# Optimization experiments

Hardware: AMD Instinct MI355X
Metric: run time of the kernel (lower is better)

The kernel has to match this reference:

```python
import jax, jax.numpy as jnp
import numpy as np

N, E, D, H1, H2 = 50000, 800000, 128, 128, 128


def setup_inputs() -> dict:
    key = jax.random.key(0)
    ks = jax.random.split(key, 9)
    s = 0.05
    return {
        "x": jax.random.normal(ks[0], (N, D), dtype=jnp.float32),
        "edge_index": jax.random.randint(ks[1], (2, E), 0, N, dtype=jnp.int64),
        "W_l1": jax.random.normal(ks[2], (D, H1), dtype=jnp.float32) * s,
        "b_l1": jnp.zeros((H1,), dtype=jnp.float32),
        "W_r1": jax.random.normal(ks[3], (D, H1), dtype=jnp.float32) * s,
        "W_l2": jax.random.normal(ks[4], (H1, H2), dtype=jnp.float32) * s,
        "b_l2": jnp.zeros((H2,), dtype=jnp.float32),
        "W_r2": jax.random.normal(ks[5], (H1, H2), dtype=jnp.float32) * s,
        "W_e": jax.random.normal(ks[6], (2 * H2, 1), dtype=jnp.float32) * s,
        "b_e": jnp.zeros((1,), dtype=jnp.float32),
    }


def _sage_conv(h, src, tgt, n_nodes, W_l, b_l, W_r):
    # PyG SAGEConv (mean aggr): out = lin_l(mean_{j in N(i)} h_j) + lin_r(h_i)
    msg = h[src]                                              # [E, F] gather
    agg = jax.ops.segment_sum(msg, tgt, num_segments=n_nodes)  # [N, F]
    cnt = jax.ops.segment_sum(jnp.ones((src.shape[0], 1), h.dtype), tgt,
                              num_segments=n_nodes)            # [N, 1]
    mean = agg / jnp.maximum(cnt, 1.0)                         # empty nbrs -> 0
    return mean @ W_l + b_l + h @ W_r


def reference(x, edge_index, W_l1, b_l1, W_r1, W_l2, b_l2, W_r2, W_e, b_e):
    src, tgt = edge_index[0], edge_index[1]
    n_nodes = x.shape[0]
    h = jax.nn.relu(_sage_conv(x, src, tgt, n_nodes, W_l1, b_l1, W_r1))
    # dropout is identity in eval mode
    h = _sage_conv(h, src, tgt, n_nodes, W_l2, b_l2, W_r2)
    z = jnp.concatenate([h[src], h[tgt]], axis=-1)  # [E, 2*H2]
    y = z @ W_e + b_e                                # [E, 1]
    return jax.nn.sigmoid(y)
```

## Files before the change

kernel.cpp:

```cpp
#include <hip/hip_runtime.h>

#define NN 50000
#define NE 800000
#define DD 128
#define BUCKETS 196
#define PB 4096
#define PBLK 196
#define EMAX 6144
#define BPAD 264
#define PACKB 6250
#define WTB 128

typedef unsigned int uint_t;
typedef unsigned short ush_t;
typedef __attribute__((ext_vector_type(8))) short short8;
typedef __attribute__((ext_vector_type(4))) float f32x4;

__device__ __forceinline__ float bflo(uint_t u) { return __uint_as_float(u << 16); }
__device__ __forceinline__ float bfhi(uint_t u) { return __uint_as_float(u & 0xffff0000u); }
__device__ __forceinline__ ush_t f2bf(float f) {
  uint_t u = __float_as_uint(f);
  u += 0x7fffu + ((u >> 16) & 1u);
  return (ush_t)(u >> 16);
}
__device__ __forceinline__ uint_t pack2(float a, float b) {
  return (uint_t)f2bf(a) | ((uint_t)f2bf(b) << 16);
}

__device__ __forceinline__ int ld_idx(const void* ei, int is64, long long i) {
  return is64 ? (int)((const long long*)ei)[i] : ((const int*)ei)[i];
}

__device__ __forceinline__ int detect64(const void* ei) {
  const unsigned long long* p = (const unsigned long long*)ei;
  unsigned long long w = p[threadIdx.x & 63];
  return __ballot((w >> 32) != 0) == 0ull ? 1 : 0;
}

__device__ __forceinline__ int block_incl_scan(int v, int tid, int* wsum) {
  int lane = tid & 63, wave = tid >> 6;
  int s = v;
#pragma unroll
  for (int off = 1; off < 64; off <<= 1) {
    int u = __shfl_up(s, off, 64);
    if (lane >= off) s += u;
  }
  if (lane == 63) wsum[wave] = s;
  __syncthreads();
  int base = 0;
  if (wave > 0) base += wsum[0];
  if (wave > 1) base += wsum[1];
  if (wave > 2) base += wsum[2];
  return base + s;
}

__global__ __launch_bounds__(256) void prep_part_k(
    const void* __restrict__ ei, int* __restrict__ bcur,
    uint_t* __restrict__ pbuf, uint_t* __restrict__ epk,
    const float* __restrict__ x, ush_t* __restrict__ xb,
    const float* __restrict__ Wl1, const float* __restrict__ Wr1,
    const float* __restrict__ Wl2, const float* __restrict__ Wr2,
    const float* __restrict__ We, const float* __restrict__ bl2,
    const float* __restrict__ be,
    ush_t* __restrict__ Wt1, float* __restrict__ uv, float* __restrict__ cc) {
  __shared__ int hist[256];
  __shared__ int basel[256];
  __shared__ int cur[256];
  __shared__ int gbase[256];
  __shared__ int wsum[4];
  __shared__ uint_t buf[PB];
  __shared__ unsigned char bbuf[PB];
  int tid = threadIdx.x;
  int blk = blockIdx.x;
  if (blk >= PBLK) {
    int blk2 = blk - PBLK;
    if (blk2 < 2) {
      const float* W = blk2 ? Wr2 : Wl2;
      int base = blk2 * 256;
      int wave = tid >> 6, lane = tid & 63;
      float e0 = We[lane], e1 = We[64 + lane];
      float f0 = We[128 + lane], f1 = We[192 + lane];
      for (int k = wave * 32; k < wave * 32 + 32; ++k) {
        float m0 = W[k * DD + lane];
        float m1 = W[k * DD + 64 + lane];
        float p = m0 * e0 + m1 * e1;
        float q = m0 * f0 + m1 * f1;
#pragma unroll
        for (int off = 32; off > 0; off >>= 1) {
          p += __shfl_down(p, off, 64);
          q += __shfl_down(q, off, 64);
        }
        if (lane == 0) {
          uv[base + k] = p;
          uv[base + 128 + k] = q;
        }
      }
      return;
    }
    if (blk2 == 2) {
      if (tid < 64) {
        int k = tid;
        float p = bl2[k] * (We[k] + We[128 + k]) +
                  bl2[k + 64] * (We[k + 64] + We[192 + k]);
#pragma unroll
        for (int off = 32; off > 0; off >>= 1) p += __shfl_down(p, off, 64);
        if (k == 0) cc[0] = p + be[0];
      }
      return;
    }
    blk2 -= 3;
    if (blk2 < PACKB) {
      int i = blk2 * 256 + tid;
      float4 v = reinterpret_cast<const float4*>(x)[i];
      uint2 o;
      o.x = pack2(v.x, v.y);
      o.y = pack2(v.z, v.w);
      reinterpret_cast<uint2*>(xb)[i] = o;
      return;
    }
    blk2 -= PACKB;
    int e = blk2 * 256 + tid;
    int col = e >> 8;
    int k = e & 255;
    float v = (k < DD) ? Wl1[k * DD + col] : Wr1[(k - DD) * DD + col];
    Wt1[col * 256 + k] = f2bf(v);
    return;
  }
  int is64 = detect64(ei);
  hist[tid] = 0;
  __syncthreads();
  long long base = (long long)blk * PB;
  uint_t pv[PB / 256];
#pragma unroll
  for (int i = 0; i < PB / 256; ++i) {
    long long e = base + i * 256 + tid;
    if (e < NE) {
      int s = ld_idx(ei, is64, e);
      int d = ld_idx(ei, is64, (long long)NE + e);
      pv[i] = ((uint_t)(d >> 8) << 24) | ((uint_t)(d & 255) << 16) | (uint_t)s;
      epk[e] = ((uint_t)d << 16) | (uint_t)s;
      atomicAdd(&hist[d >> 8], 1);
    } else {
      pv[i] = 0xFFFFFFFFu;
    }
  }
  __syncthreads();
  int hv = hist[tid];
  int incl = block_incl_scan(hv, tid, wsum);
  basel[tid] = incl - hv;
  cur[tid] = incl - hv;
  if (hv > 0) gbase[tid] = atomicAdd(&bcur[tid], hv);
  __syncthreads();
#pragma unroll
  for (int i = 0; i < PB / 256; ++i) {
    uint_t p = pv[i];
    if (p != 0xFFFFFFFFu) {
      int b = p >> 24;
      int r = atomicAdd(&cur[b], 1);
      buf[r] = p & 0xFFFFFFu;
      bbuf[r] = (unsigned char)b;
    }
  }
  __syncthreads();
  int total = basel[255] + hist[255];
  for (int j = tid; j < total; j += 256) {
    int b = bbuf[j];
    int slot = gbase[b] + (j - basel[b]);
    if (slot < EMAX) pbuf[(size_t)b * EMAX + slot] = buf[j];
  }
}

__global__ __launch_bounds__(256) void csr_k(const uint_t* __restrict__ pbuf,
                                             const int* __restrict__ bcur,
                                             int* __restrict__ offsets,
                                             int* __restrict__ srclist) {
  __shared__ int cnt[256];
  __shared__ int scur[256];
  __shared__ int wsum[4];
  __shared__ int sgb, scnt, stot;
  __shared__ uint_t ebuf[EMAX];
  int tid = threadIdx.x;
  int b = blockIdx.x;
  int v = 0;
  if (tid < BUCKETS) {
    v = bcur[tid];
    if (v > EMAX) v = EMAX;
  }
  int incl = block_incl_scan(v, tid, wsum);
  if (tid == b) { sgb = incl - v; scnt = v; }
  if (tid == BUCKETS - 1) stot = incl;
  cnt[tid] = 0;
  __syncthreads();
  int gb = sgb;
  int ecnt = scnt;
  for (int j = tid; j < ecnt; j += 256) {
    uint_t e = pbuf[(size_t)b * EMAX + j];
    ebuf[j] = e;
    atomicAdd(&cnt[(e >> 16) & 255], 1);
  }
  __syncthreads();
  int c = cnt[tid];
  int incl2 = block_incl_scan(c, tid, wsum);
  int ex = incl2 - c;
  scur[tid] = ex;
  int node = b * 256 + tid;
  if (node < NN) offsets[node] = gb + ex;
  if (b == BUCKETS - 1 && tid == 0) offsets[NN] = stot;
  __syncthreads();
  for (int j = tid; j < ecnt; j += 256) {
    uint_t e = ebuf[j];
    int p = atomicAdd(&scur[(e >> 16) & 255], 1);
    srclist[gb + p] = (int)(e & 0xFFFFu);
  }
}

__global__ __launch_bounds__(256) void agg_k(const ush_t* __restrict__ featb,
                                             const int* __restrict__ srclist,
                                             const int* __restrict__ offsets,
                                             ush_t* __restrict__ meanb) {
  int t = blockIdx.x * 256 + threadIdx.x;
  int node = t >> 4;
  int lane = t & 15;
  int f = lane << 3;
  int beg = offsets[node];
  int end = offsets[node + 1];
  float a0 = 0.f, a1 = 0.f, a2 = 0.f, a3 = 0.f, a4 = 0.f, a5 = 0.f, a6 = 0.f, a7 = 0.f;
  for (int c = beg; c < end; c += 16) {
    int idx = c + lane;
    int sl = (idx < end) ? srclist[idx] : 0;
    int m = min(16, end - c);
    int jj = 0;
    for (; jj + 4 <= m; jj += 4) {
      int s0 = __shfl(sl, jj, 16);
      int s1 = __shfl(sl, jj + 1, 16);
      int s2 = __shfl(sl, jj + 2, 16);
      int s3 = __shfl(sl, jj + 3, 16);
      uint4 v0 = *reinterpret_cast<const uint4*>(featb + (size_t)s0 * DD + f);
      uint4 v1 = *reinterpret_cast<const uint4*>(featb + (size_t)s1 * DD + f);
      uint4 v2 = *reinterpret_cast<const uint4*>(featb + (size_t)s2 * DD + f);
      uint4 v3 = *reinterpret_cast<const uint4*>(featb + (size_t)s3 * DD + f);
      a0 += bflo(v0.x); a1 += bfhi(v0.x); a2 += bflo(v0.y); a3 += bfhi(v0.y);
      a4 += bflo(v0.z); a5 += bfhi(v0.z); a6 += bflo(v0.w); a7 += bfhi(v0.w);
      a0 += bflo(v1.x); a1 += bfhi(v1.x); a2 += bflo(v1.y); a3 += bfhi(v1.y);
      a4 += bflo(v1.z); a5 += bfhi(v1.z); a6 += bflo(v1.w); a7 += bfhi(v1.w);
      a0 += bflo(v2.x); a1 += bfhi(v2.x); a2 += bflo(v2.y); a3 += bfhi(v2.y);
      a4 += bflo(v2.z); a5 += bfhi(v2.z); a6 += bflo(v2.w); a7 += bfhi(v2.w);
      a0 += bflo(v3.x); a1 += bfhi(v3.x); a2 += bflo(v3.y); a3 += bfhi(v3.y);
      a4 += bflo(v3.z); a5 += bfhi(v3.z); a6 += bflo(v3.w); a7 += bfhi(v3.w);
    }
    for (; jj < m; ++jj) {
      int s = __shfl(sl, jj, 16);
      uint4 v = *reinterpret_cast<const uint4*>(featb + (size_t)s * DD + f);
      a0 += bflo(v.x); a1 += bfhi(v.x); a2 += bflo(v.y); a3 += bfhi(v.y);
      a4 += bflo(v.z); a5 += bfhi(v.z); a6 += bflo(v.w); a7 += bfhi(v.w);
    }
  }
  float inv = 1.0f / fmaxf((float)(end - beg), 1.0f);
  uint4 o;
  o.x = pack2(a0 * inv, a1 * inv);
  o.y = pack2(a2 * inv, a3 * inv);
  o.z = pack2(a4 * inv, a5 * inv);
  o.w = pack2(a6 * inv, a7 * inv);
  *reinterpret_cast<uint4*>(meanb + (size_t)node * DD + f) = o;
}

#define MFMA_CORE(A0PTR, A1PTR, WTPTR)                                         \
  int tid = threadIdx.x;                                                       \
  int lane = tid & 63;                                                         \
  int wave = tid >> 6;                                                         \
  int n15 = lane & 15, quad = lane >> 4;                                       \
  int nb = blockIdx.x * 64;                                                    \
  for (int it = 0; it < 16; ++it) {                                            \
    int i = it * 256 + tid;                                                    \
    int col = i >> 5, c = i & 31;                                              \
    *reinterpret_cast<short8*>(&sB[col * BPAD + c * 8]) =                      \
        reinterpret_cast<const short8*>(WTPTR)[i];                             \
  }                                                                            \
  __syncthreads();                                                             \
  int row = nb + wave * 16 + n15;                                              \
  int arow = (row < NN) ? row : (NN - 1);                                      \
  const ush_t* a0 = A0PTR + (size_t)arow * DD;                                 \
  const ush_t* a1 = A1PTR + (size_t)arow * DD;                                 \
  f32x4 acc[8];                                                                \
  _Pragma("unroll")                                                            \
  for (int t = 0; t < 8; ++t) acc[t] = (f32x4){0.f, 0.f, 0.f, 0.f};           \
  _Pragma("unroll")                                                            \
  for (int c = 0; c < 8; ++c) {                                                \
    const ush_t* ap = (c < 4) ? (a0 + c * 32 + quad * 8)                       \
                              : (a1 + (c - 4) * 32 + quad * 8);                \
    short8 af = *reinterpret_cast<const short8*>(ap);                          \
    int kb = c * 32 + quad * 8;                                                \
    _Pragma("unroll")                                                          \
    for (int t = 0; t < 8; ++t) {                                              \
      short8 bf = *reinterpret_cast<const short8*>(&sB[(t * 16 + n15) * BPAD + kb]); \
      acc[t] = __builtin_amdgcn_mfma_f32_16x16x32_bf16(af, bf, acc[t], 0, 0, 0); \
    }                                                                          \
  }

__global__ __launch_bounds__(256, 2) void sage_l1(
    const ush_t* __restrict__ meanb, const ush_t* __restrict__ xb,
    const ush_t* __restrict__ Wt1, const float* __restrict__ bl,
    const float* __restrict__ uv, float2* __restrict__ t12,
    float2* __restrict__ r12) {
  __shared__ ush_t sB[128 * BPAD];
  MFMA_CORE(meanb, xb, Wt1)
  float p1[4] = {0.f, 0.f, 0.f, 0.f};
  float p2[4] = {0.f, 0.f, 0.f, 0.f};
  float q1[4] = {0.f, 0.f, 0.f, 0.f};
  float q2[4] = {0.f, 0.f, 0.f, 0.f};
#pragma unroll
  for (int t = 0; t < 8; ++t) {
    int col = t * 16 + n15;
    float b = bl[col];
    float U1 = uv[col];
    float U2 = uv[128 + col];
    float V1 = uv[256 + col];
    float V2 = uv[384 + col];
#pragma unroll
    for (int reg = 0; reg < 4; ++reg) {
      float h = fmaxf(acc[t][reg] + b, 0.f);
      p1[reg] += h * U1;
      p2[reg] += h * U2;
      q1[reg] += h * V1;
      q2[reg] += h * V2;
    }
  }
#pragma unroll
  for (int reg = 0; reg < 4; ++reg) {
    float a1 = p1[reg], a2 = p2[reg], b1 = q1[reg], b2 = q2[reg];
    for (int off = 8; off > 0; off >>= 1) {
      a1 += __shfl_down(a1, off, 16);
      a2 += __shfl_down(a2, off, 16);
      b1 += __shfl_down(b1, off, 16);
      b2 += __shfl_down(b2, off, 16);
    }
    int r = nb + wave * 16 + quad * 4 + reg;
    if (n15 == 0 && r < NN) {
      t12[r] = make_float2(a1, a2);
      r12[r] = make_float2(b1, b2);
    }
  }
}

__global__ __launch_bounds__(256) void agg2s_k(const float2* __restrict__ t12,
                                               const int* __restrict__ srclist,
                                               const int* __restrict__ offsets,
                                               const float2* __restrict__ r12,
                                               float2* __restrict__ s12) {
  int t = blockIdx.x * 256 + threadIdx.x;
  int node = t >> 4;
  int lane = t & 15;
  int beg = offsets[node];
  int end = offsets[node + 1];
  float sx = 0.f, sy = 0.f;
  for (int c = beg + lane; c < end; c += 16) {
    int s = srclist[c];
    float2 v = t12[s];
    sx += v.x;
    sy += v.y;
  }
  for (int off = 8; off > 0; off >>= 1) {
    sx += __shfl_down(sx, off, 16);
    sy += __shfl_down(sy, off, 16);
  }
  if (lane == 0) {
    float inv = 1.0f / fmaxf((float)(end - beg), 1.0f);
    float2 r = r12[node];
    s12[node] = make_float2(sx * inv + r.x, sy * inv + r.y);
  }
}

__global__ __launch_bounds__(256) void edge_k(const uint_t* __restrict__ epk,
                                              const float2* __restrict__ s12,
                                              const float* __restrict__ cc,
                                              float* __restrict__ out) {
  int e = blockIdx.x * 256 + threadIdx.x;
  uint_t p = epk[e];
  float2 a = s12[p & 0xFFFFu];
  float2 b = s12[p >> 16];
  float v = a.x + b.y + cc[0];
  out[e] = 1.0f / (1.0f + __expf(-v));
}

extern "C" void kernel_launch(void* const* d_in, const int* in_sizes, int n_in,
                              void* d_out, int out_size, void* d_ws, size_t ws_size,
                              hipStream_t stream) {
  const float* x   = (const float*)d_in[0];
  const void*  ei  = d_in[1];
  const float* Wl1 = (const float*)d_in[2];
  const float* bl1 = (const float*)d_in[3];
  const float* Wr1 = (const float*)d_in[4];
  const float* Wl2 = (const float*)d_in[5];
  const float* bl2 = (const float*)d_in[6];
  const float* Wr2 = (const float*)d_in[7];
  const float* We  = (const float*)d_in[8];
  const float* be  = (const float*)d_in[9];
  float* out = (float*)d_out;

  int* bcur    = (int*)d_ws;
  int* offsets = bcur + 256;
  uint_t* epk  = (uint_t*)(offsets + 50004);
  uint_t* pbuf = epk + NE;
  int* srclist = (int*)(pbuf + (size_t)BUCKETS * EMAX);
  ush_t* xb    = (ush_t*)(srclist + NE);
  ush_t* meanb = xb + (size_t)NN * DD;
  float2* t12  = (float2*)(meanb + (size_t)NN * DD);
  float2* r12  = t12 + NN;
  float2* s12  = r12 + NN;
  ush_t* Wt1   = (ush_t*)(s12 + NN);
  float* uv    = (float*)(Wt1 + 32768);
  float* cc    = uv + 512;

  hipMemsetAsync(bcur, 0, 256 * sizeof(int), stream);
  prep_part_k<<<PBLK + 3 + PACKB + WTB, 256, 0, stream>>>(
      ei, bcur, pbuf, epk, x, xb, Wl1, Wr1, Wl2, Wr2, We, bl2, be, Wt1, uv, cc);
  csr_k<<<BUCKETS, 256, 0, stream>>>(pbuf, bcur, offsets, srclist);

  agg_k<<<(NN * 16) / 256, 256, 0, stream>>>(xb, srclist, offsets, meanb);

  int gemm_blocks = (NN + 63) / 64;
  sage_l1<<<gemm_blocks, 256, 0, stream>>>(meanb, xb, Wt1, bl1, uv, t12, r12);

  agg2s_k<<<(NN * 16) / 256, 256, 0, stream>>>(t12, srclist, offsets, r12, s12);

  edge_k<<<NE / 256, 256, 0, stream>>>(epk, s12, cc, out);
}
```

Baseline: 183.3 us.

## Fuse layer-1 neighbor aggregation into the MFMA GEMM kernel via shared memory

The separate mean-aggregation kernel is merged into the layer-1 GEMM kernel. Each block gathers neighbor means for its 64 rows into shared memory and feeds them straight to MFMA, so the bf16 mean buffer is never written to or read back from global memory and one launch goes away. The padded weight tile layout is replaced by an XOR-swizzled layout to avoid LDS bank conflicts. The cost is more shared memory per block (about 80KB), which may lower occupancy, and the gather phase now runs with only four rows per 16-lane group inside the GEMM block, so it has less parallelism to hide memory latency.

```diff
diff --git a/kernel.cpp b/kernel.cpp
--- a/kernel.cpp
+++ b/kernel.cpp
@@ -7,7 +7,6 @@
 #define PB 4096
 #define PBLK 196
 #define EMAX 6144
-#define BPAD 264
 #define PACKB 6250
 #define WTB 128
 
@@ -214,96 +213,110 @@
   }
 }
 
-__global__ __launch_bounds__(256) void agg_k(const ush_t* __restrict__ featb,
-                                             const int* __restrict__ srclist,
-                                             const int* __restrict__ offsets,
-                                             ush_t* __restrict__ meanb) {
-  int t = blockIdx.x * 256 + threadIdx.x;
-  int node = t >> 4;
-  int lane = t & 15;
-  int f = lane << 3;
-  int beg = offsets[node];
-  int end = offsets[node + 1];
-  float a0 = 0.f, a1 = 0.f, a2 = 0.f, a3 = 0.f, a4 = 0.f, a5 = 0.f, a6 = 0.f, a7 = 0.f;
-  for (int c = beg; c < end; c += 16) {
-    int idx = c + lane;
-    int sl = (idx < end) ? srclist[idx] : 0;
-    int m = min(16, end - c);
-    int jj = 0;
-    for (; jj + 4 <= m; jj += 4) {
-      int s0 = __shfl(sl, jj, 16);
-      int s1 = __shfl(sl, jj + 1, 16);
-      int s2 = __shfl(sl, jj + 2, 16);
-      int s3 = __shfl(sl, jj + 3, 16);
-      uint4 v0 = *reinterpret_cast<const uint4*>(featb + (size_t)s0 * DD + f);
-      uint4 v1 = *reinterpret_cast<const uint4*>(featb + (size_t)s1 * DD + f);
-      uint4 v2 = *reinterpret_cast<const uint4*>(featb + (size_t)s2 * DD + f);
-      uint4 v3 = *reinterpret_cast<const uint4*>(featb + (size_t)s3 * DD + f);
-      a0 += bflo(v0.x); a1 += bfhi(v0.x); a2 += bflo(v0.y); a3 += bfhi(v0.y);
-      a4 += bflo(v0.z); a5 += bfhi(v0.z); a6 += bflo(v0.w); a7 += bfhi(v0.w);
-      a0 += bflo(v1.x); a1 += bfhi(v1.x); a2 += bflo(v1.y); a3 += bfhi(v1.y);
-      a4 += bflo(v1.z); a5 += bfhi(v1.z); a6 += bflo(v1.w); a7 += bfhi(v1.w);
-      a0 += bflo(v2.x); a1 += bfhi(v2.x); a2 += bflo(v2.y); a3 += bfhi(v2.y);
-      a4 += bflo(v2.z); a5 += bfhi(v2.z); a6 += bflo(v2.w); a7 += bfhi(v2.w);
-      a0 += bflo(v3.x); a1 += bfhi(v3.x); a2 += bflo(v3.y); a3 += bfhi(v3.y);
-      a4 += bflo(v3.z); a5 += bfhi(v3.z); a6 += bflo(v3.w); a7 += bfhi(v3.w);
-    }
-    for (; jj < m; ++jj) {
-      int s = __shfl(sl, jj, 16);
-      uint4 v = *reinterpret_cast<const uint4*>(featb + (size_t)s * DD + f);
-      a0 += bflo(v.x); a1 += bfhi(v.x); a2 += bflo(v.y); a3 += bfhi(v.y);
-      a4 += bflo(v.z); a5 += bfhi(v.z); a6 += bflo(v.w); a7 += bfhi(v.w);
-    }
-  }
-  float inv = 1.0f / fmaxf((float)(end - beg), 1.0f);
-  uint4 o;
-  o.x = pack2(a0 * inv, a1 * inv);
-  o.y = pack2(a2 * inv, a3 * inv);
-  o.z = pack2(a4 * inv, a5 * inv);
-  o.w = pack2(a6 * inv, a7 * inv);
-  *reinterpret_cast<uint4*>(meanb + (size_t)node * DD + f) = o;
-}
-
-#define MFMA_CORE(A0PTR, A1PTR, WTPTR)                                         \
-  int tid = threadIdx.x;                                                       \
-  int lane = tid & 63;                                                         \
-  int wave = tid >> 6;                                                         \
-  int n15 = lane & 15, quad = lane >> 4;                                       \
-  int nb = blockIdx.x * 64;                                                    \
-  for (int it = 0; it < 16; ++it) {                                            \
-    int i = it * 256 + tid;                                                    \
-    int col = i >> 5, c = i & 31;                                              \
-    *reinterpret_cast<short8*>(&sB[col * BPAD + c * 8]) =                      \
-        reinterpret_cast<const short8*>(WTPTR)[i];                             \
-  }                                                                            \
-  __syncthreads();                                                             \
-  int row = nb + wave * 16 + n15;                                              \
-  int arow = (row < NN) ? row : (NN - 1);                                      \
-  const ush_t* a0 = A0PTR + (size_t)arow * DD;                                 \
-  const ush_t* a1 = A1PTR + (size_t)arow * DD;                                 \
-  f32x4 acc[8];                                                                \
-  _Pragma("unroll")                                                            \
-  for (int t = 0; t < 8; ++t) acc[t] = (f32x4){0.f, 0.f, 0.f, 0.f};           \
-  _Pragma("unroll")                                                            \
-  for (int c = 0; c < 8; ++c) {                                                \
-    const ush_t* ap = (c < 4) ? (a0 + c * 32 + quad * 8)                       \
-                              : (a1 + (c - 4) * 32 + quad * 8);                \
-    short8 af = *reinterpret_cast<const short8*>(ap);                          \
-    int kb = c * 32 + quad * 8;                                                \
-    _Pragma("unroll")                                                          \
-    for (int t = 0; t < 8; ++t) {                                              \
-      short8 bf = *reinterpret_cast<const short8*>(&sB[(t * 16 + n15) * BPAD + kb]); \
-      acc[t] = __builtin_amdgcn_mfma_f32_16x16x32_bf16(af, bf, acc[t], 0, 0, 0); \
-    }                                                                          \
-  }
-
-__global__ __launch_bounds__(256, 2) void sage_l1(
-    const ush_t* __restrict__ meanb, const ush_t* __restrict__ xb,
-    const ush_t* __restrict__ Wt1, const float* __restrict__ bl,
-    const float* __restrict__ uv, float2* __restrict__ t12,
-    float2* __restrict__ r12) {
-  __shared__ ush_t sB[128 * BPAD];
-  MFMA_CORE(meanb, xb, Wt1)
+__global__ __launch_bounds__(256, 2) void agg_l1_k(
+    const ush_t* __restrict__ xb, const int* __restrict__ srclist,
+    const int* __restrict__ offsets, const ush_t* __restrict__ Wt1,
+    const float* __restrict__ bl, const float* __restrict__ uv,
+    float2* __restrict__ t12, float2* __restrict__ r12) {
+  __shared__ ush_t sB[128 * 256];
+  __shared__ ush_t sM[64 * 128];
+  int tid = threadIdx.x;
+  int lane = tid & 63;
+  int wave = tid >> 6;
+  int n15 = lane & 15, quad = lane >> 4;
+  int nb = blockIdx.x * 64;
+
+#pragma unroll
+  for (int it = 0; it < 16; ++it) {
+    int i = it * 256 + tid;
+    int col = i >> 5, c2 = i & 31;
+    int byt = (col << 9) + (c2 << 4);
+    byt ^= (col & 7) << 4;
+    *reinterpret_cast<short8*>(reinterpret_cast<char*>(sB) + byt) =
+        reinterpret_cast<const short8*>(Wt1)[i];
+  }
+
+  int g = tid >> 4, lane16 = tid & 15;
+  int f = lane16 << 3;
+  for (int p = 0; p < 4; ++p) {
+    int lr = p * 16 + g;
+    int node = nb + lr;
+    float a0 = 0.f, a1 = 0.f, a2 = 0.f, a3 = 0.f;
+    float a4 = 0.f, a5 = 0.f, a6 = 0.f, a7 = 0.f;
+    int beg = 0, end = 0;
+    if (node < NN) {
+      beg = offsets[node];
+      end = offsets[node + 1];
+    }
+    for (int c = beg; c < end; c += 16) {
+      int idx = c + lane16;
+      int sl = (idx < end) ? srclist[idx] : 0;
+      int m = min(16, end - c);
+      int jj = 0;
+      for (; jj + 4 <= m; jj += 4) {
+        int s0 = __shfl(sl, jj, 16);
+        int s1 = __shfl(sl, jj + 1, 16);
+        int s2 = __shfl(sl, jj + 2, 16);
+        int s3 = __shfl(sl, jj + 3, 16);
+        uint4 v0 = *reinterpret_cast<const uint4*>(xb + (size_t)s0 * DD + f);
+        uint4 v1 = *reinterpret_cast<const uint4*>(xb + (size_t)s1 * DD + f);
+        uint4 v2 = *reinterpret_cast<const uint4*>(xb + (size_t)s2 * DD + f);
+        uint4 v3 = *reinterpret_cast<const uint4*>(xb + (size_t)s3 * DD + f);
+        a0 += bflo(v0.x); a1 += bfhi(v0.x); a2 += bflo(v0.y); a3 += bfhi(v0.y);
+        a4 += bflo(v0.z); a5 += bfhi(v0.z); a6 += bflo(v0.w); a7 += bfhi(v0.w);
+        a0 += bflo(v1.x); a1 += bfhi(v1.x); a2 += bflo(v1.y); a3 += bfhi(v1.y);
+        a4 += bflo(v1.z); a5 += bfhi(v1.z); a6 += bflo(v1.w); a7 += bfhi(v1.w);
+        a0 += bflo(v2.x); a1 += bfhi(v2.x); a2 += bflo(v2.y); a3 += bfhi(v2.y);
+        a4 += bflo(v2.z); a5 += bfhi(v2.z); a6 += bflo(v2.w); a7 += bfhi(v2.w);
+        a0 += bflo(v3.x); a1 += bfhi(v3.x); a2 += bflo(v3.y); a3 += bfhi(v3.y);
+        a4 += bflo(v3.z); a5 += bfhi(v3.z); a6 += bflo(v3.w); a7 += bfhi(v3.w);
+      }
+      for (; jj < m; ++jj) {
+        int s = __shfl(sl, jj, 16);
+        uint4 v = *reinterpret_cast<const uint4*>(xb + (size_t)s * DD + f);
+        a0 += bflo(v.x); a1 += bfhi(v.x); a2 += bflo(v.y); a3 += bfhi(v.y);
+        a4 += bflo(v.z); a5 += bfhi(v.z); a6 += bflo(v.w); a7 += bfhi(v.w);
+      }
+    }
+    float inv = 1.0f / fmaxf((float)(end - beg), 1.0f);
+    uint4 o;
+    o.x = pack2(a0 * inv, a1 * inv);
+    o.y = pack2(a2 * inv, a3 * inv);
+    o.z = pack2(a4 * inv, a5 * inv);
+    o.w = pack2(a6 * inv, a7 * inv);
+    int byt = (lr << 8) + (lane16 << 4);
+    byt ^= (lr & 7) << 4;
+    *reinterpret_cast<uint4*>(reinterpret_cast<char*>(sM) + byt) = o;
+  }
+  __syncthreads();
+
+  int row = nb + wave * 16 + n15;
+  int arow = (row < NN) ? row : (NN - 1);
+  const ush_t* a1p = xb + (size_t)arow * DD;
+  int lr = wave * 16 + n15;
+  f32x4 acc[8];
+#pragma unroll
+  for (int t = 0; t < 8; ++t) acc[t] = (f32x4){0.f, 0.f, 0.f, 0.f};
+#pragma unroll
+  for (int c = 0; c < 8; ++c) {
+    short8 af;
+    if (c < 4) {
+      int byt = (lr << 8) + (c << 6) + (quad << 4);
+      byt ^= (lr & 7) << 4;
+      af = *reinterpret_cast<const short8*>(reinterpret_cast<const char*>(sM) + byt);
+    } else {
+      af = *reinterpret_cast<const short8*>(a1p + (c - 4) * 32 + quad * 8);
+    }
+#pragma unroll
+    for (int t = 0; t < 8; ++t) {
+      int brow = t * 16 + n15;
+      int byt = (brow << 9) + (c << 6) + (quad << 4);
+      byt ^= (brow & 7) << 4;
+      short8 bf = *reinterpret_cast<const short8*>(reinterpret_cast<const char*>(sB) + byt);
+      acc[t] = __builtin_amdgcn_mfma_f32_16x16x32_bf16(af, bf, acc[t], 0, 0, 0);
+    }
+  }
+
   float p1[4] = {0.f, 0.f, 0.f, 0.f};
   float p2[4] = {0.f, 0.f, 0.f, 0.f};
   float q1[4] = {0.f, 0.f, 0.f, 0.f};
@@ -403,8 +416,7 @@
   uint_t* pbuf = epk + NE;
   int* srclist = (int*)(pbuf + (size_t)BUCKETS * EMAX);
   ush_t* xb    = (ush_t*)(srclist + NE);
-  ush_t* meanb = xb + (size_t)NN * DD;
-  float2* t12  = (float2*)(meanb + (size_t)NN * DD);
+  float2* t12  = (float2*)(xb + (size_t)NN * DD);
   float2* r12  = t12 + NN;
   float2* s12  = r12 + NN;
   ush_t* Wt1   = (ush_t*)(s12 + NN);
@@ -416,10 +428,9 @@
       ei, bcur, pbuf, epk, x, xb, Wl1, Wr1, Wl2, Wr2, We, bl2, be, Wt1, uv, cc);
   csr_k<<<BUCKETS, 256, 0, stream>>>(pbuf, bcur, offsets, srclist);
 
-  agg_k<<<(NN * 16) / 256, 256, 0, stream>>>(xb, srclist, offsets, meanb);
-
   int gemm_blocks = (NN + 63) / 64;
-  sage_l1<<<gemm_blocks, 256, 0, stream>>>(meanb, xb, Wt1, bl1, uv, t12, r12);
+  agg_l1_k<<<gemm_blocks, 256, 0, stream>>>(xb, srclist, offsets, Wt1, bl1, uv,
+                                            t12, r12);
 
   agg2s_k<<<(NN * 16) / 256, 256, 0, stream>>>(t12, srclist, offsets, r12, s12);
 
```

New measurement: 191.0 us. +4.2%, slower.
